# Performance work log

Measured on AMD Instinct MI355X. Metric: run time of the kernel, lower is better.

## Reference

```python
import jax, jax.numpy as jnp
import numpy as np

NEG_SLOPE = 0.01  # torch nn.LeakyReLU default

B, N, IN_F, OUT_F, HEADS = 4, 2048, 512, 512, 8
D = OUT_F // HEADS  # 64


def setup_inputs() -> dict:
    key = jax.random.key(0)
    ks = jax.random.split(key, 4)
    X = jax.random.normal(ks[0], (B, N, IN_F), dtype=jnp.float32)
    W_v = jax.random.normal(ks[1], (IN_F, D), dtype=jnp.float32) * (IN_F ** -0.5)
    b_v = jnp.zeros((D,), dtype=jnp.float32)
    W_q = jax.random.normal(ks[2], (D, HEADS), dtype=jnp.float32) * (D ** -0.5)
    b_q = jnp.zeros((HEADS,), dtype=jnp.float32)
    W_k = jax.random.normal(ks[3], (D, HEADS), dtype=jnp.float32) * (D ** -0.5)
    b_k = jnp.zeros((HEADS,), dtype=jnp.float32)
    return {"X": X, "W_v": W_v, "b_v": b_v, "W_q": W_q, "b_q": b_q, "W_k": W_k, "b_k": b_k}


def reference(X, W_v, b_v, W_q, b_q, W_k, b_k):
    # V: (B, N, D)
    V = X @ W_v + b_v
    # per-node, per-head scalar scores: (B, N, H) -> (B, H, N)
    Q = jnp.swapaxes(V @ W_q + b_q, 1, 2)
    K = jnp.swapaxes(V @ W_k + b_k, 1, 2)
    # A[b,h,i,j] = leaky_relu(Q[b,h,j] + K[b,h,i])  (broadcast outer-sum)
    A = jax.nn.leaky_relu(Q[:, :, None, :] + K[:, :, :, None], negative_slope=NEG_SLOPE)
    A = jax.nn.softmax(A, axis=-1)  # dropout = identity in eval mode
    # H[b,i,h,f] = sum_j A[b,h,i,j] V[b,j,f]
    H = jnp.einsum('bhij,bjf->bihf', A, V)
    return H.reshape(H.shape[0], H.shape[1], -1)  # (B, N, H*D)
```

## Files before the change

kernel.cpp:

```cpp
#include <hip/hip_runtime.h>

#define BB   4
#define NN   2048
#define INF  512
#define HH   8
#define DD   64
#define BH   (BB*HH)
#define NCK  16
#define CKS  128


__global__ __launch_bounds__(256) void k_vq(
    const float* __restrict__ X, const float* __restrict__ Wv,
    const float* __restrict__ bv,
    const float* __restrict__ Wq, const float* __restrict__ bq,
    const float* __restrict__ Wk, const float* __restrict__ bk,
    float* __restrict__ V, float* __restrict__ ksg,
    unsigned long long* __restrict__ qk64)
{
  __shared__ float Ws[2][64][68];
  __shared__ float red[128][16];
  __shared__ float Vs[32][65];
  const int t  = threadIdx.x;
  const int kh = t >> 7;
  const int u  = t & 127;
  const int tc = u & 15;
  const int rg = u >> 4;
  const int r0 = blockIdx.x * 32;
  const int k0 = kh * 256;
  float acc[4][4];
  #pragma unroll
  for (int r = 0; r < 4; r++)
    #pragma unroll
    for (int c = 0; c < 4; c++) acc[r][c] = 0.f;

  for (int kc = 0; kc < 256; kc += 64) {
    __syncthreads();
    #pragma unroll
    for (int i = 0; i < 8; i++) {
      const int e4 = u + i * 128;
      const int k  = e4 >> 4;
      const int n4 = (e4 & 15) * 4;
      *(float4*)(&Ws[kh][k][n4]) =
          *(const float4*)(Wv + (size_t)(k0 + kc + k) * DD + n4);
    }
    __syncthreads();
    const float* xp = X + (size_t)(r0 + rg * 4) * INF + k0 + kc;
    #pragma unroll 4
    for (int kk = 0; kk < 64; kk += 4) {
      float4 xr[4];
      #pragma unroll
      for (int r = 0; r < 4; r++)
        xr[r] = *(const float4*)(xp + (size_t)r * INF + kk);
      #pragma unroll
      for (int j = 0; j < 4; j++) {
        const float4 w4 = *(const float4*)(&Ws[kh][kk + j][tc * 4]);
        #pragma unroll
        for (int r = 0; r < 4; r++) {
          const float x = (j == 0) ? xr[r].x : (j == 1) ? xr[r].y
                        : (j == 2) ? xr[r].z : xr[r].w;
          acc[r][0] += x * w4.x;  acc[r][1] += x * w4.y;
          acc[r][2] += x * w4.z;  acc[r][3] += x * w4.w;
        }
      }
    }
  }

  __syncthreads();
  if (kh == 1) {
    #pragma unroll
    for (int r = 0; r < 4; r++)
      *(float4*)(&red[u][r * 4]) = *(const float4*)(&acc[r][0]);
  }
  __syncthreads();
  if (kh == 0) {
    const float4 bb = *(const float4*)(bv + tc * 4);
    #pragma unroll
    for (int r = 0; r < 4; r++) {
      const float4 p = *(const float4*)(&red[u][r * 4]);
      float4 o;
      o.x = acc[r][0] + p.x + bb.x;  o.y = acc[r][1] + p.y + bb.y;
      o.z = acc[r][2] + p.z + bb.z;  o.w = acc[r][3] + p.w + bb.w;
      *(float4*)(V + (size_t)(r0 + rg * 4 + r) * DD + tc * 4) = o;
      Vs[rg * 4 + r][tc * 4]     = o.x;  Vs[rg * 4 + r][tc * 4 + 1] = o.y;
      Vs[rg * 4 + r][tc * 4 + 2] = o.z;  Vs[rg * 4 + r][tc * 4 + 3] = o.w;
    }
  }
  __syncthreads();

  const int row = t >> 3;
  const int h   = t & 7;
  float sq = bq[h], sk = bk[h];
  #pragma unroll 8
  for (int dd = 0; dd < DD; dd++) {
    const float v = Vs[row][dd];
    sq += v * Wq[dd * HH + h];
    sk += v * Wk[dd * HH + h];
  }
  const int grow = r0 + row;
  const int b = grow >> 11, n = grow & (NN - 1);
  const int bh = b * HH + h;
  ksg[bh * NN + n] = sk;
  unsigned uo = __float_as_uint(sq);
  uo = (uo & 0x80000000u) ? ~uo : (uo | 0x80000000u);
  qk64[(size_t)bh * NN + n] = ((unsigned long long)uo << 32) | (unsigned)n;
}

__global__ __launch_bounds__(256) void k_rank(
    const unsigned long long* __restrict__ qk64,
    float* __restrict__ sqs, unsigned short* __restrict__ idxg)
{
  __shared__ __align__(16) unsigned long long keys[NN];
  __shared__ int cnt[4][256];
  const int t  = threadIdx.x;
  const int bh = blockIdx.x >> 3;
  const int jq = t & 63;
  const int kq = t >> 6;
  const unsigned long long* __restrict__ kb = qk64 + (size_t)bh * NN;

  {
    const ulonglong2* __restrict__ g2 = (const ulonglong2*)kb;
    ulonglong2* s2 = (ulonglong2*)keys;
    #pragma unroll
    for (int x = 0; x < 4; x++) s2[t + 256 * x] = g2[t + 256 * x];
  }
  __syncthreads();

  const int jg = ((blockIdx.x & 7) << 8) | (jq << 2);
  const unsigned long long kj0 = keys[jg];
  const unsigned long long kj1 = keys[jg + 1];
  const unsigned long long kj2 = keys[jg + 2];
  const unsigned long long kj3 = keys[jg + 3];

  const ulonglong2* __restrict__ k2 = (const ulonglong2*)(keys + kq * 512);
  int c0 = 0, c1 = 0, c2 = 0, c3 = 0;
  #pragma unroll 8
  for (int l = 0; l < 256; l++) {
    const ulonglong2 kk = k2[l];
    c0 += (kk.x < kj0) + (kk.y < kj0);
    c1 += (kk.x < kj1) + (kk.y < kj1);
    c2 += (kk.x < kj2) + (kk.y < kj2);
    c3 += (kk.x < kj3) + (kk.y < kj3);
  }
  cnt[kq][0 * 64 + jq] = c0;
  cnt[kq][1 * 64 + jq] = c1;
  cnt[kq][2 * 64 + jq] = c2;
  cnt[kq][3 * 64 + jq] = c3;
  __syncthreads();

  if (kq == 0) {
    #pragma unroll
    for (int u = 0; u < 4; u++) {
      const int rank = cnt[0][u * 64 + jq] + cnt[1][u * 64 + jq]
                     + cnt[2][u * 64 + jq] + cnt[3][u * 64 + jq];
      const unsigned long long kj = keys[jg + u];
      const unsigned uo = (unsigned)(kj >> 32);
      const unsigned ur = (uo & 0x80000000u) ? (uo & 0x7fffffffu) : ~uo;
      sqs [bh * NN + rank] = __uint_as_float(ur);
      idxg[bh * NN + rank] = (unsigned short)(jg + u);
    }
  }
}

__global__ __launch_bounds__(256) void k_csum(
    const float* __restrict__ sqs, const unsigned short* __restrict__ idxg,
    const float* __restrict__ V,
    float* __restrict__ S1g, float* __restrict__ S2g,
    float* __restrict__ SL1, float* __restrict__ SL2)
{
  __shared__ float ss1[4][64], ss2[4][64];
  __shared__ float sl1[4], sl2[4];
  const int t  = threadIdx.x;
  const int bh = blockIdx.x >> 4;
  const int ck = blockIdx.x & 15;
  const int d  = t & 63, g = t >> 6;
  const int r0 = ck * CKS + g * 32;
  const float* Vb  = V + (size_t)(bh >> 3) * NN * DD;
  const float* sqb = sqs + bh * NN;
  const unsigned short* ib = idxg + bh * NN;
  float a1 = 0.f, a2 = 0.f, s1 = 0.f, s2 = 0.f;
  #pragma unroll 8
  for (int rr = 0; rr < 32; rr++) {
    const int r = r0 + rr;
    const float qv = sqb[r];
    const float e1 = __expf(qv), e2 = __expf(0.01f * qv);
    const float v  = Vb[(size_t)ib[r] * DD + d];
    a1 += e1 * v;  a2 += e2 * v;  s1 += e1;  s2 += e2;
  }
  ss1[g][d] = a1;  ss2[g][d] = a2;
  if (d == 0) { sl1[g] = s1;  sl2[g] = s2; }
  __syncthreads();
  if (g == 0) {
    S1g[(bh*NCK + ck)*64 + d] = ss1[0][d]+ss1[1][d]+ss1[2][d]+ss1[3][d];
    S2g[(bh*NCK + ck)*64 + d] = ss2[0][d]+ss2[1][d]+ss2[2][d]+ss2[3][d];
    if (d == 0) {
      SL1[bh*NCK + ck] = sl1[0]+sl1[1]+sl1[2]+sl1[3];
      SL2[bh*NCK + ck] = sl2[0]+sl2[1]+sl2[2]+sl2[3];
    }
  }
}

__global__ __launch_bounds__(256) void k_out2(
    const float* __restrict__ sqs, const unsigned short* __restrict__ idxg,
    const float* __restrict__ V, const float* __restrict__ ksg,
    const float* __restrict__ S1g, const float* __restrict__ S2g,
    const float* __restrict__ SL1, const float* __restrict__ SL2,
    float* __restrict__ out)
{
  __shared__ float P1l[CKS + 1][64];
  __shared__ float P2l[CKS + 1][64];
  __shared__ float sqc[CKS];
  __shared__ float Ll1[CKS + 1], Ll2[CKS + 1];
  __shared__ __align__(16) unsigned char scr[12304];
  __shared__ int nwl;

  float (*ss1)[64] = (float(*)[64])scr;
  float (*ss2)[64] = (float(*)[64])(scr + 1024);
  float* sl1 = (float*)(scr + 2048);
  float* sl2 = (float*)(scr + 2064);
  unsigned short* wl = (unsigned short*)scr;
  float* kwl = (float*)(scr + 4096);

  const int t  = threadIdx.x;
  const int bh = blockIdx.x >> 4;
  const int ck = blockIdx.x & 15;
  const int d  = t & 63, g = t >> 6;
  const int r0 = ck * CKS + g * 32;
  const int b  = bh >> 3, h = bh & 7;
  const float* Vb  = V + (size_t)b * NN * DD;
  const float* sqb = sqs + bh * NN;
  const unsigned short* ib = idxg + bh * NN;

  if (t < CKS) sqc[t] = sqb[ck * CKS + t];
  if (t == 0) nwl = 0;

  float a1 = 0.f, a2 = 0.f, s1 = 0.f, s2 = 0.f;
  #pragma unroll 8
  for (int rr = 0; rr < 32; rr++) {
    const int r = r0 + rr;
    const float qv = sqb[r];
    const float e1 = __expf(qv), e2 = __expf(0.01f * qv);
    const float v  = Vb[(size_t)ib[r] * DD + d];
    P1l[g * 32 + rr][d] = v;
    a1 += e1 * v;  a2 += e2 * v;  s1 += e1;  s2 += e2;
  }
  ss1[g][d] = a1;  ss2[g][d] = a2;
  if (d == 0) { sl1[g] = s1;  sl2[g] = s2; }
  __syncthreads();
  float o1 = 0.f, o2 = 0.f, lo1 = 0.f, lo2 = 0.f;
  for (int gg = 0; gg < g; gg++) { o1 += ss1[gg][d]; o2 += ss2[gg][d]; lo1 += sl1[gg]; lo2 += sl2[gg]; }

  a1 = o1;  a2 = o2;  s1 = lo1;  s2 = lo2;
  #pragma unroll 8
  for (int rr = 0; rr < 32; rr++) {
    const int row = g * 32 + rr;
    const float qv = sqb[r0 + rr];
    const float e1 = __expf(qv), e2 = __expf(0.01f * qv);
    const float v  = P1l[row][d];
    P1l[row][d] = a1;
    P2l[row][d] = a2;
    if (d == 0) { Ll1[row] = s1;  Ll2[row] = s2; }
    a1 += e1 * v;  a2 += e2 * v;  s1 += e1;  s2 += e2;
  }
  if (g == 3) {
    P1l[CKS][d] = a1;  P2l[CKS][d] = a2;
    if (d == 0) { Ll1[CKS] = s1;  Ll2[CKS] = s2; }
  }
  __syncthreads();

  float of1 = 0.f, of2 = 0.f, t1 = 0.f, t2 = 0.f;
  float so1 = 0.f, so2 = 0.f, lt1 = 0.f, lt2 = 0.f;
  #pragma unroll
  for (int c2 = 0; c2 < NCK; c2++) {
    const float v1 = S1g[(bh*NCK + c2)*64 + d];
    const float v2 = S2g[(bh*NCK + c2)*64 + d];
    const float w1 = SL1[bh*NCK + c2];
    const float w2 = SL2[bh*NCK + c2];
    t1 += v1;  t2 += v2;  lt1 += w1;  lt2 += w2;
    if (c2 < ck) { of1 += v1; of2 += v2; so1 += w1; so2 += w2; }
  }
  const float qlo = ck ? sqb[ck * CKS - 1] : -__builtin_inff();
  const float qhi = (ck < NCK - 1) ? sqc[CKS - 1] : __builtin_inff();

  const float* kb = ksg + bh * NN;
  #pragma unroll
  for (int s = 0; s < 8; s++) {
    const int i = t + 256 * s;
    const float kv = kb[i];
    const float tt = -kv;
    if (qlo <= tt && tt < qhi) {
      const int slot = atomicAdd(&nwl, 1);
      wl[slot]  = (unsigned short)i;
      kwl[slot] = kv;
    }
  }
  __syncthreads();

  const int n = nwl;
  for (int e = g; e < n; e += 4) {
    const int i = wl[e];
    const float kv = kwl[e];
    const float tt = -kv;
    const unsigned long long b0 = __ballot(sqc[d] <= tt);
    const unsigned long long b1 = __ballot(sqc[64 + d] <= tt);
    const int loc = __popcll(b0) + __popcll(b1);
    const float p1v = of1 + P1l[loc][d];
    const float p2v = of2 + P2l[loc][d];
    const float q1v = so1 + Ll1[loc];
    const float q2v = so2 + Ll2[loc];
    const float ek  = __expf(kv);
    const float ek2 = __expf(0.01f * kv);
    const float num = ek * (t1  - p1v) + ek2 * p2v;
    const float den = ek * (lt1 - q1v) + ek2 * q2v;
    out[((size_t)(b * NN + i)) * (HH * DD) + h * DD + d] = num / den;
  }
}

extern "C" void kernel_launch(void* const* d_in, const int* in_sizes, int n_in,
                              void* d_out, int out_size, void* d_ws, size_t ws_size,
                              hipStream_t stream)
{
  (void)in_sizes; (void)n_in; (void)out_size; (void)ws_size;
  const float* X  = (const float*)d_in[0];
  const float* Wv = (const float*)d_in[1];
  const float* bv = (const float*)d_in[2];
  const float* Wq = (const float*)d_in[3];
  const float* bq = (const float*)d_in[4];
  const float* Wk = (const float*)d_in[5];
  const float* bk = (const float*)d_in[6];
  float* out = (float*)d_out;

  float* w = (float*)d_ws;
  float* V     = w;  w += (size_t)BB*NN*DD;
  float* ksg   = w;  w += BH*NN;
  unsigned short* idxg = (unsigned short*)w;  w += BH*NN/2;
  float* S1g   = w;  w += (size_t)BH*NCK*DD;
  float* S2g   = w;  w += (size_t)BH*NCK*DD;
  float* SL1   = w;  w += BH*NCK;
  float* SL2   = w;  w += BH*NCK;
  float* sqs   = w;  w += BH*NN;
  unsigned long long* qk64 = (unsigned long long*)w;  w += BH*NN*2;

  k_vq   <<<256, 256, 0, stream>>>(X, Wv, bv, Wq, bq, Wk, bk, V, ksg, qk64);
  k_rank <<<BH*8, 256, 0, stream>>>(qk64, sqs, idxg);
  k_csum <<<BH*NCK, 256, 0, stream>>>(sqs, idxg, V, S1g, S2g, SL1, SL2);
  k_out2 <<<BH*NCK, 256, 0, stream>>>(sqs, idxg, V, ksg, S1g, S2g, SL1, SL2, out);
}
```

Measured before the change: 136.5 us.

## Rebalance V-projection K-split and rank tiles, hoist ballot loads in output

```diff
diff --git a/kernel.cpp b/kernel.cpp
--- a/kernel.cpp
+++ b/kernel.cpp
@@ -18,45 +18,44 @@
     float* __restrict__ V, float* __restrict__ ksg,
     unsigned long long* __restrict__ qk64)
 {
-  __shared__ float Ws[2][64][68];
-  __shared__ float red[128][16];
+  __shared__ float Ws[4][64][68];
+  __shared__ float red[3][32][64];
   __shared__ float Vs[32][65];
   const int t  = threadIdx.x;
-  const int kh = t >> 7;
-  const int u  = t & 127;
+  const int kh = t >> 6;
+  const int u  = t & 63;
   const int tc = u & 15;
-  const int rg = u >> 4;
+  const int rw = u >> 4;
   const int r0 = blockIdx.x * 32;
-  const int k0 = kh * 256;
-  float acc[4][4];
-  #pragma unroll
-  for (int r = 0; r < 4; r++)
+  float acc[8][4];
+  #pragma unroll
+  for (int r = 0; r < 8; r++)
     #pragma unroll
     for (int c = 0; c < 4; c++) acc[r][c] = 0.f;
 
-  for (int kc = 0; kc < 256; kc += 64) {
+  for (int kc = 0; kc < 128; kc += 64) {
     __syncthreads();
     #pragma unroll
-    for (int i = 0; i < 8; i++) {
-      const int e4 = u + i * 128;
+    for (int i = 0; i < 16; i++) {
+      const int e4 = u + i * 64;
       const int k  = e4 >> 4;
       const int n4 = (e4 & 15) * 4;
       *(float4*)(&Ws[kh][k][n4]) =
-          *(const float4*)(Wv + (size_t)(k0 + kc + k) * DD + n4);
+          *(const float4*)(Wv + (size_t)(kh * 128 + kc + k) * DD + n4);
     }
     __syncthreads();
-    const float* xp = X + (size_t)(r0 + rg * 4) * INF + k0 + kc;
-    #pragma unroll 4
+    const float* xp = X + (size_t)(r0 + rw * 8) * INF + kh * 128 + kc;
+    #pragma unroll 2
     for (int kk = 0; kk < 64; kk += 4) {
-      float4 xr[4];
+      float4 xr[8];
       #pragma unroll
-      for (int r = 0; r < 4; r++)
+      for (int r = 0; r < 8; r++)
         xr[r] = *(const float4*)(xp + (size_t)r * INF + kk);
       #pragma unroll
       for (int j = 0; j < 4; j++) {
         const float4 w4 = *(const float4*)(&Ws[kh][kk + j][tc * 4]);
         #pragma unroll
-        for (int r = 0; r < 4; r++) {
+        for (int r = 0; r < 8; r++) {
           const float x = (j == 0) ? xr[r].x : (j == 1) ? xr[r].y
                         : (j == 2) ? xr[r].z : xr[r].w;
           acc[r][0] += x * w4.x;  acc[r][1] += x * w4.y;
@@ -67,23 +66,26 @@
   }
 
   __syncthreads();
-  if (kh == 1) {
-    #pragma unroll
-    for (int r = 0; r < 4; r++)
-      *(float4*)(&red[u][r * 4]) = *(const float4*)(&acc[r][0]);
+  if (kh > 0) {
+    #pragma unroll
+    for (int r = 0; r < 8; r++)
+      #pragma unroll
+      for (int c = 0; c < 4; c++)
+        red[kh - 1][r * 4 + c][u] = acc[r][c];
   }
   __syncthreads();
   if (kh == 0) {
     const float4 bb = *(const float4*)(bv + tc * 4);
     #pragma unroll
-    for (int r = 0; r < 4; r++) {
-      const float4 p = *(const float4*)(&red[u][r * 4]);
+    for (int r = 0; r < 8; r++) {
       float4 o;
-      o.x = acc[r][0] + p.x + bb.x;  o.y = acc[r][1] + p.y + bb.y;
-      o.z = acc[r][2] + p.z + bb.z;  o.w = acc[r][3] + p.w + bb.w;
-      *(float4*)(V + (size_t)(r0 + rg * 4 + r) * DD + tc * 4) = o;
-      Vs[rg * 4 + r][tc * 4]     = o.x;  Vs[rg * 4 + r][tc * 4 + 1] = o.y;
-      Vs[rg * 4 + r][tc * 4 + 2] = o.z;  Vs[rg * 4 + r][tc * 4 + 3] = o.w;
+      o.x = acc[r][0] + red[0][r*4+0][u] + red[1][r*4+0][u] + red[2][r*4+0][u] + bb.x;
+      o.y = acc[r][1] + red[0][r*4+1][u] + red[1][r*4+1][u] + red[2][r*4+1][u] + bb.y;
+      o.z = acc[r][2] + red[0][r*4+2][u] + red[1][r*4+2][u] + red[2][r*4+2][u] + bb.z;
+      o.w = acc[r][3] + red[0][r*4+3][u] + red[1][r*4+3][u] + red[2][r*4+3][u] + bb.w;
+      *(float4*)(V + (size_t)(r0 + rw * 8 + r) * DD + tc * 4) = o;
+      Vs[rw * 8 + r][tc * 4]     = o.x;  Vs[rw * 8 + r][tc * 4 + 1] = o.y;
+      Vs[rw * 8 + r][tc * 4 + 2] = o.z;  Vs[rw * 8 + r][tc * 4 + 3] = o.w;
     }
   }
   __syncthreads();
@@ -111,11 +113,12 @@
     float* __restrict__ sqs, unsigned short* __restrict__ idxg)
 {
   __shared__ __align__(16) unsigned long long keys[NN];
-  __shared__ int cnt[4][256];
-  const int t  = threadIdx.x;
-  const int bh = blockIdx.x >> 3;
-  const int jq = t & 63;
-  const int kq = t >> 6;
+  __shared__ int cnt[8][256];
+  const int t    = threadIdx.x;
+  const int bh   = blockIdx.x >> 3;
+  const int slab = blockIdx.x & 7;
+  const int jq   = t & 31;
+  const int kq   = t >> 5;
   const unsigned long long* __restrict__ kb = qk64 + (size_t)bh * NN;
 
   {
@@ -126,39 +129,35 @@
   }
   __syncthreads();
 
-  const int jg = ((blockIdx.x & 7) << 8) | (jq << 2);
-  const unsigned long long kj0 = keys[jg];
-  const unsigned long long kj1 = keys[jg + 1];
-  const unsigned long long kj2 = keys[jg + 2];
-  const unsigned long long kj3 = keys[jg + 3];
-
-  const ulonglong2* __restrict__ k2 = (const ulonglong2*)(keys + kq * 512);
-  int c0 = 0, c1 = 0, c2 = 0, c3 = 0;
-  #pragma unroll 8
-  for (int l = 0; l < 256; l++) {
+  const int jg = (slab << 8) | (jq << 3);
+  unsigned long long kj[8];
+  #pragma unroll
+  for (int u2 = 0; u2 < 8; u2++) kj[u2] = keys[jg + u2];
+
+  int c[8] = {0, 0, 0, 0, 0, 0, 0, 0};
+  const ulonglong2* __restrict__ k2 = (const ulonglong2*)(keys + kq * 256);
+  #pragma unroll 8
+  for (int l = 0; l < 128; l++) {
     const ulonglong2 kk = k2[l];
-    c0 += (kk.x < kj0) + (kk.y < kj0);
-    c1 += (kk.x < kj1) + (kk.y < kj1);
-    c2 += (kk.x < kj2) + (kk.y < kj2);
-    c3 += (kk.x < kj3) + (kk.y < kj3);
-  }
-  cnt[kq][0 * 64 + jq] = c0;
-  cnt[kq][1 * 64 + jq] = c1;
-  cnt[kq][2 * 64 + jq] = c2;
-  cnt[kq][3 * 64 + jq] = c3;
-  __syncthreads();
-
-  if (kq == 0) {
-    #pragma unroll
-    for (int u = 0; u < 4; u++) {
-      const int rank = cnt[0][u * 64 + jq] + cnt[1][u * 64 + jq]
-                     + cnt[2][u * 64 + jq] + cnt[3][u * 64 + jq];
-      const unsigned long long kj = keys[jg + u];
-      const unsigned uo = (unsigned)(kj >> 32);
-      const unsigned ur = (uo & 0x80000000u) ? (uo & 0x7fffffffu) : ~uo;
-      sqs [bh * NN + rank] = __uint_as_float(ur);
-      idxg[bh * NN + rank] = (unsigned short)(jg + u);
-    }
+    #pragma unroll
+    for (int u2 = 0; u2 < 8; u2++)
+      c[u2] += (kk.x < kj[u2]) + (kk.y < kj[u2]);
+  }
+  #pragma unroll
+  for (int u2 = 0; u2 < 8; u2++) cnt[kq][u2 * 32 + jq] = c[u2];
+  __syncthreads();
+
+  {
+    const int jl = t;
+    const int ci = (jl & 7) * 32 + (jl >> 3);
+    int rank = 0;
+    #pragma unroll
+    for (int q = 0; q < 8; q++) rank += cnt[q][ci];
+    const unsigned long long kj2 = keys[(slab << 8) | jl];
+    const unsigned uo = (unsigned)(kj2 >> 32);
+    const unsigned ur = (uo & 0x80000000u) ? (uo & 0x7fffffffu) : ~uo;
+    sqs [bh * NN + rank] = __uint_as_float(ur);
+    idxg[bh * NN + rank] = (unsigned short)((slab << 8) | jl);
   }
 }
 
@@ -296,13 +295,15 @@
   }
   __syncthreads();
 
+  const float sq0 = sqc[d];
+  const float sq1 = sqc[64 + d];
   const int n = nwl;
   for (int e = g; e < n; e += 4) {
     const int i = wl[e];
     const float kv = kwl[e];
     const float tt = -kv;
-    const unsigned long long b0 = __ballot(sqc[d] <= tt);
-    const unsigned long long b1 = __ballot(sqc[64 + d] <= tt);
+    const unsigned long long b0 = __ballot(sq0 <= tt);
+    const unsigned long long b1 = __ballot(sq1 <= tt);
     const int loc = __popcll(b0) + __popcll(b1);
     const float p1v = of1 + P1l[loc][d];
     const float p2v = of2 + P2l[loc][d];
```

Result: faster. 131.8 us, median of 2 (-3.5%).
